# Performance work log

Measured on AMD Instinct MI355X. Metric: run time of the kernel, lower is better.

The kernel has to match this reference:

```python
import jax, jax.numpy as jnp
import numpy as np

NUM_OPS = 100_000
NUM_MACH = 512
H = 128
OPF = 6
MF = 2
L = 2
N_PREC = 800_000
N_CHALF = 800_000  # compat edges per direction
EPS = 1e-5


def setup_inputs() -> dict:
    key = jax.random.key(0)
    ks = jax.random.split(key, 20)
    op_features = jax.random.normal(ks[0], (NUM_OPS, OPF), dtype=jnp.float32)
    machine_features = jax.random.normal(ks[1], (NUM_MACH, MF), dtype=jnp.float32)
    prec_src = jax.random.randint(ks[2], (N_PREC,), 0, NUM_OPS, dtype=jnp.int32)
    prec_tgt = jax.random.randint(ks[3], (N_PREC,), 0, NUM_OPS, dtype=jnp.int32)
    precedence_edges = jnp.stack([prec_src, prec_tgt])  # [2, N_PREC]
    op_idx = jax.random.randint(ks[4], (N_CHALF,), 0, NUM_OPS, dtype=jnp.int32)
    m_idx = jax.random.randint(ks[5], (N_CHALF,), 0, NUM_MACH, dtype=jnp.int32)
    # bidirectional pairs in unified node space (machines offset by NUM_OPS)
    src = jnp.concatenate([op_idx, m_idx + NUM_OPS])
    tgt = jnp.concatenate([m_idx + NUM_OPS, op_idx])
    compatibility_edges = jnp.stack([src, tgt])  # [2, 2*N_CHALF]
    s = 0.05
    op_emb_W = jax.random.normal(ks[6], (H, OPF), dtype=jnp.float32) * s
    op_emb_b = jnp.zeros((H,), jnp.float32)
    mach_emb_W = jax.random.normal(ks[7], (H, MF), dtype=jnp.float32) * s
    mach_emb_b = jnp.zeros((H,), jnp.float32)
    prec_W = jax.random.normal(ks[8], (L, H, H), dtype=jnp.float32) * s
    prec_b = jax.random.normal(ks[9], (L, H), dtype=jnp.float32) * s
    compat_W = jax.random.normal(ks[10], (L, H, H), dtype=jnp.float32) * s
    compat_b = jax.random.normal(ks[11], (L, H), dtype=jnp.float32) * s
    op_ln_g = jnp.ones((L, H), jnp.float32)
    op_ln_b = jnp.zeros((L, H), jnp.float32)
    mach_ln_g = jnp.ones((L, H), jnp.float32)
    mach_ln_b = jnp.zeros((L, H), jnp.float32)
    return dict(op_features=op_features, machine_features=machine_features,
                precedence_edges=precedence_edges, compatibility_edges=compatibility_edges,
                op_emb_W=op_emb_W, op_emb_b=op_emb_b, mach_emb_W=mach_emb_W, mach_emb_b=mach_emb_b,
                prec_W=prec_W, prec_b=prec_b, compat_W=compat_W, compat_b=compat_b,
                op_ln_g=op_ln_g, op_ln_b=op_ln_b, mach_ln_g=mach_ln_g, mach_ln_b=mach_ln_b)


def _layer_norm(x, g, b):
    mu = jnp.mean(x, axis=-1, keepdims=True)
    var = jnp.mean(jnp.square(x - mu), axis=-1, keepdims=True)
    return (x - mu) * jax.lax.rsqrt(var + EPS) * g + b


def _scatter_mean(vals, idx, mask, n):
    # vals [E,H], idx [E], mask [E] bool (or None); mean over incoming edges, count clamped >= 1
    if mask is not None:
        vals = jnp.where(mask[:, None], vals, 0.0)
        idx = jnp.where(mask, idx, 0)
        ones = mask.astype(vals.dtype)
    else:
        ones = jnp.ones(idx.shape, vals.dtype)
    sums = jax.ops.segment_sum(vals, idx, num_segments=n)
    cnts = jax.ops.segment_sum(ones, idx, num_segments=n)
    return sums / jnp.maximum(cnts, 1.0)[:, None]


def _forward(op_features, machine_features, precedence_edges, compatibility_edges,
             op_emb_W, op_emb_b, mach_emb_W, mach_emb_b,
             prec_W, prec_b, compat_W, compat_b,
             op_ln_g, op_ln_b, mach_ln_g, mach_ln_b):
    num_ops = op_features.shape[0]
    num_mach = machine_features.shape[0]
    op_emb = op_features @ op_emb_W.T + op_emb_b
    mach_emb = machine_features @ mach_emb_W.T + mach_emb_b

    p_src, p_tgt = precedence_edges[0], precedence_edges[1]
    c_src, c_tgt = compatibility_edges[0], compatibility_edges[1]
    op2m = (c_src < num_ops) & (c_tgt >= num_ops)
    m2o = (c_src >= num_ops) & (c_tgt < num_ops)
    o2m_src = jnp.where(op2m, c_src, 0)
    o2m_tgt = jnp.where(op2m, c_tgt - num_ops, 0)
    m2o_src = jnp.where(m2o, c_src - num_ops, 0)
    m2o_tgt = jnp.where(m2o, c_tgt, 0)

    for l in range(L):
        # precedence (op -> op): linear-then-gather == gather-then-linear
        op_t = op_emb @ prec_W[l].T + prec_b[l]            # [num_ops, H]
        op_emb_prec = _scatter_mean(op_t[p_src], p_tgt, None, num_ops)
        # compatibility, shared linear for both directions
        op_c = op_emb @ compat_W[l].T + compat_b[l]        # [num_ops, H]
        mach_c = mach_emb @ compat_W[l].T + compat_b[l]    # [num_mach, H]
        mach_emb_compat = _scatter_mean(op_c[o2m_src], o2m_tgt, op2m, num_mach)
        op_emb_compat = _scatter_mean(mach_c[m2o_src], m2o_tgt, m2o, num_ops)
        op_emb = _layer_norm(op_emb + op_emb_prec + op_emb_compat, op_ln_g[l], op_ln_b[l])
        mach_emb = _layer_norm(mach_emb + mach_emb_compat, mach_ln_g[l], mach_ln_b[l])
    return op_emb, mach_emb


def reference(op_features, machine_features, precedence_edges, compatibility_edges,
              op_emb_W, op_emb_b, mach_emb_W, mach_emb_b,
              prec_W, prec_b, compat_W, compat_b,
              op_ln_g, op_ln_b, mach_ln_g, mach_ln_b):
    return _forward(op_features, machine_features, precedence_edges, compatibility_edges,
                    op_emb_W, op_emb_b, mach_emb_W, mach_emb_b,
                    prec_W, prec_b, compat_W, compat_b,
                    op_ln_g, op_ln_b, mach_ln_g, mach_ln_b)
```

## Files before the change

### kernel.cpp

```cpp
#include <hip/hip_runtime.h>
#include <hip/hip_bf16.h>

#define NUM_OPS   100000
#define NUM_MACH  512
#define HDIM      128
#define P1        100352
#define NHIST     200704
#define NBLK      196
#define NCOARSE   784
#define NBC       256
#define NBM       256
#define MHWORDS   (NUM_MACH * NBM)
#define NBLK_M    128
#define NBLK_T    (NBLK + NBLK_M)

typedef short short8 __attribute__((ext_vector_type(8)));
typedef unsigned short ushort8 __attribute__((ext_vector_type(8)));
typedef float floatx4 __attribute__((ext_vector_type(4)));

__device__ __forceinline__ unsigned short f2bf(float f) {
    unsigned u = __float_as_uint(f);
    unsigned r = (u + 0x7FFFu + ((u >> 16) & 1u)) >> 16;
    return (unsigned short)r;
}
__device__ __forceinline__ float bf2f(unsigned short u) {
    return __uint_as_float(((unsigned)u) << 16);
}

__global__ void k_prep(const float* __restrict__ Fo, const float* __restrict__ Fm,
                       const float* __restrict__ Wo, const float* __restrict__ bo,
                       const float* __restrict__ Wm, const float* __restrict__ bm,
                       const float* __restrict__ Wp, const float* __restrict__ Wc,
                       unsigned short* __restrict__ op_ebf,
                       float* __restrict__ mach_emb, unsigned short* __restrict__ mach_ebf,
                       unsigned short* __restrict__ Wb) {
    int idx = blockIdx.x * blockDim.x + threadIdx.x;
    if (idx < NUM_OPS * HDIM) {
        int r = idx >> 7, h = idx & 127;
        const float* f = Fo + (size_t)r * 6;
        const float* w = Wo + (size_t)h * 6;
        float s = bo[h];
#pragma unroll
        for (int i = 0; i < 6; ++i) s += f[i] * w[i];
        op_ebf[idx] = f2bf(s);
        return;
    }
    idx -= NUM_OPS * HDIM;
    if (idx < NUM_MACH * HDIM) {
        int r = idx >> 7, h = idx & 127;
        const float* f = Fm + (size_t)r * 2;
        const float* w = Wm + (size_t)h * 2;
        float s = bm[h] + f[0] * w[0] + f[1] * w[1];
        mach_emb[idx] = s;
        mach_ebf[idx] = f2bf(s);
        return;
    }
    idx -= NUM_MACH * HDIM;
    if (idx < 2 * 128 * 256) {
        int l = idx >> 15, h = (idx >> 8) & 127, k = idx & 255;
        float v = (k < 128) ? Wp[(size_t)l * 16384 + h * 128 + k]
                            : Wc[(size_t)l * 16384 + h * 128 + (k - 128)];
        Wb[idx] = f2bf(v);
    }
}

__global__ __launch_bounds__(256) void k_front(const int* __restrict__ prec_e, int nprec,
                                               const int* __restrict__ comp_e, int E, int M,
                                               int* __restrict__ chist_bh,
                                               int* __restrict__ mach_bh) {
    __shared__ int hc[NCOARSE];
    __shared__ int hm[NUM_MACH];
    for (int i = threadIdx.x; i < NCOARSE; i += 256) hc[i] = 0;
    for (int i = threadIdx.x; i < NUM_MACH; i += 256) hm[i] = 0;
    __syncthreads();
    int NT = nprec + E;
    int ch = (NT + NBC - 1) / NBC;
    int i0 = blockIdx.x * ch, i1 = min(NT, i0 + ch);
    for (int i = i0 + threadIdx.x; i < i1; i += 256) {
        int key;
        if (i < nprec) key = prec_e[nprec + i];
        else {
            int e = i - nprec;
            key = P1 + comp_e[e];
            atomicAdd(&hm[comp_e[E + e] - M], 1);
        }
        atomicAdd(&hc[key >> 8], 1);
    }
    __syncthreads();
    for (int i = threadIdx.x; i < NCOARSE; i += 256)
        chist_bh[i * NBC + blockIdx.x] = hc[i];
    for (int i = threadIdx.x; i < NUM_MACH; i += 256)
        mach_bh[i * NBC + blockIdx.x] = hm[i];
}

__global__ __launch_bounds__(256) void k_cfill(const int* __restrict__ prec_e, int nprec,
                                               const int* __restrict__ comp_e, int E, int M,
                                               const int* __restrict__ scan,
                                               int* __restrict__ pairs) {
    __shared__ int cur[NCOARSE];
    for (int i = threadIdx.x; i < NCOARSE; i += 256) cur[i] = scan[i * NBC + blockIdx.x];
    __syncthreads();
    int NT = nprec + E;
    int ch = (NT + NBC - 1) / NBC;
    int i0 = blockIdx.x * ch, i1 = min(NT, i0 + ch);
    for (int i = i0 + threadIdx.x; i < i1; i += 256) {
        int key, val;
        if (i < nprec) { key = prec_e[nprec + i]; val = prec_e[i]; }
        else { int e = i - nprec; key = P1 + comp_e[e]; val = comp_e[E + e] - M; }
        int pos = atomicAdd(&cur[key >> 8], 1);
        pairs[pos] = (val << 8) | (key & 255);
    }
}

__global__ __launch_bounds__(256) void k_blocksum(const int* __restrict__ arr, int* __restrict__ partial) {
    __shared__ int sh[256];
    int b = blockIdx.x, t = threadIdx.x;
    int4 v = *(const int4*)(arr + b * 1024 + t * 4);
    sh[t] = v.x + v.y + v.z + v.w;
    __syncthreads();
    for (int o = 128; o; o >>= 1) { if (t < o) sh[t] += sh[t + o]; __syncthreads(); }
    if (!t) partial[b] = sh[0];
}

__global__ __launch_bounds__(256) void k_scanpart(const int* __restrict__ partial,
                                                  int* __restrict__ block_off) {
    __shared__ int sh[256];
    int t = threadIdx.x;
    int seg0 = blockIdx.x ? NBLK : 0;
    int n    = blockIdx.x ? NBLK_M : NBLK;
    int v = (t < n) ? partial[seg0 + t] : 0;
    sh[t] = v; __syncthreads();
    for (int o = 1; o < 256; o <<= 1) {
        int x = (t >= o) ? sh[t - o] : 0; __syncthreads();
        sh[t] += x; __syncthreads();
    }
    if (t < n) block_off[seg0 + t] = sh[t] - v;
}

__global__ __launch_bounds__(256) void k_scanwrite(const int* __restrict__ arr,
                                                   const int* __restrict__ block_off,
                                                   int* __restrict__ rs) {
    __shared__ int sh[256];
    int b = blockIdx.x, t = threadIdx.x;
    int base_i = b * 1024 + t * 4;
    int4 v = *(const int4*)(arr + base_i);
    int tsum = v.x + v.y + v.z + v.w;
    sh[t] = tsum; __syncthreads();
    for (int o = 1; o < 256; o <<= 1) {
        int x = (t >= o) ? sh[t - o] : 0; __syncthreads();
        sh[t] += x; __syncthreads();
    }
    int off = block_off[b] + sh[t] - tsum;
    int4 r; r.x = off; r.y = off + v.x; r.z = off + v.x + v.y; r.w = off + v.x + v.y + v.z;
    *(int4*)(rs + base_i) = r;
}

__global__ __launch_bounds__(256) void k_finefill(const int* __restrict__ scans, int NT,
                                                  const int* __restrict__ pairs,
                                                  int* __restrict__ rs,
                                                  int* __restrict__ bucket_all,
                                                  const int* __restrict__ comp_e, int E, int M,
                                                  int* __restrict__ bucket_mach,
                                                  int* __restrict__ mach_rs) {
    int t = threadIdx.x;
    if (blockIdx.x < NCOARSE) {
        __shared__ int hh[256];
        __shared__ int ex[256];
        __shared__ int cu[256];
        int b = blockIdx.x;
        int s = scans[b * NBC];
        int e = (b == NCOARSE - 1) ? NT : scans[(b + 1) * NBC];
        hh[t] = 0;
        __syncthreads();
        for (int i = s + t; i < e; i += 256) atomicAdd(&hh[pairs[i] & 255], 1);
        __syncthreads();
        int v = hh[t];
        ex[t] = v; __syncthreads();
        for (int o = 1; o < 256; o <<= 1) {
            int x = (t >= o) ? ex[t - o] : 0; __syncthreads();
            ex[t] += x; __syncthreads();
        }
        int start = s + ex[t] - v;
        rs[b * 256 + t] = start;
        cu[t] = start;
        __syncthreads();
        for (int i = s + t; i < e; i += 256) {
            int p = pairs[i];
            int pos = atomicAdd(&cu[p & 255], 1);
            bucket_all[pos] = ((unsigned)p) >> 8;
        }
    } else {
        __shared__ int cur[NUM_MACH];
        int blk = blockIdx.x - NCOARSE;
        const int* moff = scans + NHIST;
        for (int i = t; i < NUM_MACH; i += 256) cur[i] = moff[i * NBM + blk];
        if (blk == 0) {
            for (int m = t; m < NUM_MACH; m += 256) mach_rs[m] = moff[m * NBM];
            if (t == 0) mach_rs[NUM_MACH] = E;
        }
        __syncthreads();
        int nprec = NT - E;
        int chNT = (NT + NBC - 1) / NBC;
        int e0 = blk * chNT - nprec;       if (e0 < 0) e0 = 0;
        int e1 = (blk + 1) * chNT - nprec; if (e1 > E) e1 = E;
        for (int e = e0 + t; e < e1; e += 256) {
            int m = comp_e[E + e] - M;
            int op = comp_e[e];
            int pos = atomicAdd(&cur[m], 1);
            bucket_mach[pos] = op;
        }
    }
}

#define ACC8(acc, v) { _Pragma("unroll") for (int k = 0; k < 8; ++k) acc[k] += bf2f((unsigned short)v[k]); }

__global__ __launch_bounds__(256) void k_aggmg(
    const unsigned short* __restrict__ op_ebf, const unsigned short* __restrict__ mach_ebf,
    const int* __restrict__ rs, const int* __restrict__ bucket_all,
    unsigned short* __restrict__ Ab, int* __restrict__ flags, int M,
    const int* __restrict__ mach_rs, const int* __restrict__ bucket_mach,
    float* __restrict__ mach_sum, int nb_agg) {
    int wave = threadIdx.x >> 6, lane = threadIdx.x & 63;
    int g = lane >> 4;
    int d = (lane & 15) * 8;

    if ((int)blockIdx.x < nb_agg) {
        int r = blockIdx.x * 4 + wave;
        if (r >= M) return;
        int sA = rs[r],      eA = rs[r + 1];
        int sB = rs[P1 + r], eB = rs[P1 + r + 1];

        float a[8], b[8];
#pragma unroll
        for (int k = 0; k < 8; ++k) { a[k] = 0.f; b[k] = 0.f; }

        int baseA = sA, baseB = sB;
        while (baseA < eA || baseB < eB) {
            int cA = (baseA < eA) ? min(64, eA - baseA) : 0;
            int cB = (baseB < eB) ? min(64, eB - baseB) : 0;
            int idxA = (lane < cA) ? bucket_all[baseA + lane] : 0;
            int idxB = (lane < cB) ? bucket_all[baseB + lane] : 0;
            int jm = max(cA, cB);
            for (int j = 0; j < jm; j += 8) {
                int j0 = j + g, j1 = j + 4 + g;
                int rA0 = __shfl(idxA, j0);
                int rA1 = __shfl(idxA, j1);
                int rB0 = __shfl(idxB, j0);
                int rB1 = __shfl(idxB, j1);
                short8 vA0 = *(const short8*)(op_ebf   + (size_t)rA0 * HDIM + d);
                short8 vA1 = *(const short8*)(op_ebf   + (size_t)rA1 * HDIM + d);
                short8 vB0 = *(const short8*)(mach_ebf + (size_t)rB0 * HDIM + d);
                short8 vB1 = *(const short8*)(mach_ebf + (size_t)rB1 * HDIM + d);
                if (j0 < cA) ACC8(a, vA0);
                if (j1 < cA) ACC8(a, vA1);
                if (j0 < cB) ACC8(b, vB0);
                if (j1 < cB) ACC8(b, vB1);
            }
            baseA += 64; baseB += 64;
        }
#pragma unroll
        for (int k = 0; k < 8; ++k) {
            a[k] += __shfl_xor(a[k], 16);
            a[k] += __shfl_xor(a[k], 32);
            b[k] += __shfl_xor(b[k], 16);
            b[k] += __shfl_xor(b[k], 32);
        }
        float pinv = 1.f / fmaxf((float)(eA - sA), 1.f);
        float cinv = 1.f / fmaxf((float)(eB - sB), 1.f);

        if (lane < 16) {
            ushort8 pa, pb;
#pragma unroll
            for (int k = 0; k < 8; ++k) { pa[k] = f2bf(a[k] * pinv); pb[k] = f2bf(b[k] * cinv); }
            *(ushort8*)(Ab + (size_t)r * 256 + d)       = pa;
            *(ushort8*)(Ab + (size_t)r * 256 + 128 + d) = pb;
        }
        if (lane == 0) flags[r] = (eA > sA ? 1 : 0) | (eB > sB ? 2 : 0);
        return;
    }

    int b2 = blockIdx.x - nb_agg;
    int m  = b2 & 511;
    int yq = b2 >> 9;
    int s0 = mach_rs[m], e0 = mach_rs[m + 1];
    float a[8];
#pragma unroll
    for (int k = 0; k < 8; ++k) a[k] = 0.f;

    for (int base = s0 + (yq * 4 + wave) * 64; base < e0; base += 1024) {
        int cnt = min(64, e0 - base);
        int idx = (lane < cnt) ? bucket_mach[base + lane] : 0;
        int j = 0;
        for (; j + 16 <= cnt; j += 16) {
            int r0 = __shfl(idx, j + g);
            int r1 = __shfl(idx, j + 4 + g);
            int r2 = __shfl(idx, j + 8 + g);
            int r3 = __shfl(idx, j + 12 + g);
            short8 v0 = *(const short8*)(op_ebf + (size_t)r0 * HDIM + d);
            short8 v1 = *(const short8*)(op_ebf + (size_t)r1 * HDIM + d);
            short8 v2 = *(const short8*)(op_ebf + (size_t)r2 * HDIM + d);
            short8 v3 = *(const short8*)(op_ebf + (size_t)r3 * HDIM + d);
            ACC8(a, v0); ACC8(a, v1); ACC8(a, v2); ACC8(a, v3);
        }
        for (; j < cnt; j += 4) {
            int jj = j + g;
            int rowi = __shfl(idx, jj);
            short8 v = *(const short8*)(op_ebf + (size_t)rowi * HDIM + d);
            if (jj < cnt) ACC8(a, v);
        }
    }
#pragma unroll
    for (int k = 0; k < 8; ++k) {
        a[k] += __shfl_xor(a[k], 16);
        a[k] += __shfl_xor(a[k], 32);
    }
    if (lane < 16) {
#pragma unroll
        for (int k = 0; k < 8; ++k)
            atomicAdd(&mach_sum[m * HDIM + d + k], a[k]);
    }
}

__global__ __launch_bounds__(256) void k_gemm_mupd(
    const unsigned short* __restrict__ Ab, const unsigned short* __restrict__ embb,
    const unsigned short* __restrict__ Wb,
    const float* __restrict__ bp, const float* __restrict__ bc,
    const int* __restrict__ flags,
    const float* __restrict__ g, const float* __restrict__ bt,
    float* __restrict__ dstf, unsigned short* __restrict__ dstb, int M, int nb_gemm,
    const float* __restrict__ mach_emb, float* __restrict__ mach_sum,
    const int* __restrict__ mach_rs,
    const float* __restrict__ Wc,
    const float* __restrict__ gm, const float* __restrict__ btm,
    float* __restrict__ mdst, unsigned short* __restrict__ mdstb) {
    if ((int)blockIdx.x >= nb_gemm) {
        __shared__ float row[HDIM];
        __shared__ float red[4];
        int m = blockIdx.x - nb_gemm, t = threadIdx.x;
        int cnt = mach_rs[m + 1] - mach_rs[m];
        float sc = (cnt > 0) ? 1.f / (float)cnt : 0.f;
        if (t < HDIM) {
            row[t] = mach_sum[m * HDIM + t] * sc;
            mach_sum[m * HDIM + t] = 0.f;
        }
        __syncthreads();
        float x = 0.f, s = 0.f, q = 0.f;
        if (t < HDIM) {
            float dot = bc[t];
            const float* w = Wc + (size_t)t * HDIM;
#pragma unroll 8
            for (int k = 0; k < HDIM; ++k) dot += row[k] * w[k];
            x = mach_emb[m * HDIM + t] + ((cnt > 0) ? dot : 0.f);
            s = x; q = x * x;
#pragma unroll
            for (int o = 32; o; o >>= 1) { s += __shfl_xor(s, o); q += __shfl_xor(q, o); }
            int wv = t >> 6;
            if ((t & 63) == 0) { red[wv * 2] = s; red[wv * 2 + 1] = q; }
        }
        __syncthreads();
        if (t < HDIM) {
            s = red[0] + red[2]; q = red[1] + red[3];
            float mu = s * (1.f / 128.f);
            float rstd = rsqrtf(fmaxf(q * (1.f / 128.f) - mu * mu, 0.f) + 1e-5f);
            float y = (x - mu) * rstd * gm[t] + btm[t];
            mdst[m * HDIM + t] = y;
            if (mdstb) mdstb[m * HDIM + t] = f2bf(y);
        }
        return;
    }

    int wave = threadIdx.x >> 6, lane = threadIdx.x & 63;
    int m0 = blockIdx.x * 64 + wave * 16;
    if (m0 >= M) return;
    int quad = lane >> 4, col = lane & 15;

    floatx4 acc[8];
#pragma unroll
    for (int t = 0; t < 8; ++t) acc[t] = (floatx4){0.f, 0.f, 0.f, 0.f};

    const short* Arow  = (const short*)(Ab + (size_t)(m0 + col) * 256);
    const short* Wbase = (const short*)Wb;

#pragma unroll
    for (int ks = 0; ks < 8; ++ks) {
        short8 a = *(const short8*)(Arow + ks * 32 + quad * 8);
#pragma unroll
        for (int t = 0; t < 8; ++t) {
            short8 b = *(const short8*)(Wbase + (size_t)(t * 16 + col) * 256 + ks * 32 + quad * 8);
            acc[t] = __builtin_amdgcn_mfma_f32_16x16x32_bf16(a, b, acc[t], 0, 0, 0);
        }
    }

    float bpv[8], bcv[8], gv[8], btv[8];
#pragma unroll
    for (int t = 0; t < 8; ++t) {
        int c = t * 16 + col;
        bpv[t] = bp[c]; bcv[t] = bc[c]; gv[t] = g[c]; btv[t] = bt[c];
    }
#pragma unroll
    for (int reg = 0; reg < 4; ++reg) {
        int r = m0 + quad * 4 + reg;
        int fl = flags[r];
        float fp = (fl & 1) ? 1.f : 0.f, fc = (fl & 2) ? 1.f : 0.f;
        float x[8]; float s = 0.f, q = 0.f;
#pragma unroll
        for (int t = 0; t < 8; ++t) {
            float v = acc[t][reg] + bf2f(embb[(size_t)r * HDIM + t * 16 + col]) + fp * bpv[t] + fc * bcv[t];
            x[t] = v; s += v; q += v * v;
        }
#pragma unroll
        for (int msk = 1; msk < 16; msk <<= 1) { s += __shfl_xor(s, msk); q += __shfl_xor(q, msk); }
        float mu = s * (1.f / 128.f);
        float rstd = rsqrtf(fmaxf(q * (1.f / 128.f) - mu * mu, 0.f) + 1e-5f);
#pragma unroll
        for (int t = 0; t < 8; ++t) {
            float y = (x[t] - mu) * rstd * gv[t] + btv[t];
            if (dstf) dstf[(size_t)r * HDIM + t * 16 + col] = y;
            if (dstb) dstb[(size_t)r * HDIM + t * 16 + col] = f2bf(y);
        }
    }
}

extern "C" void kernel_launch(void* const* d_in, const int* in_sizes, int n_in,
                              void* d_out, int out_size, void* d_ws, size_t ws_size,
                              hipStream_t stream) {
    const float* op_feat    = (const float*)d_in[0];
    const float* m_feat     = (const float*)d_in[1];
    const int*   prec_e     = (const int*)d_in[2];
    const int*   comp_e     = (const int*)d_in[3];
    const float* op_emb_W   = (const float*)d_in[4];
    const float* op_emb_b   = (const float*)d_in[5];
    const float* mach_emb_W = (const float*)d_in[6];
    const float* mach_emb_b = (const float*)d_in[7];
    const float* prec_W     = (const float*)d_in[8];
    const float* prec_b     = (const float*)d_in[9];
    const float* compat_W   = (const float*)d_in[10];
    const float* compat_b   = (const float*)d_in[11];
    const float* op_ln_g    = (const float*)d_in[12];
    const float* op_ln_b    = (const float*)d_in[13];
    const float* mach_ln_g  = (const float*)d_in[14];
    const float* mach_ln_b  = (const float*)d_in[15];
    float* out = (float*)d_out;

    const int M = NUM_OPS, NM = NUM_MACH;
    const int nprec = in_sizes[2] / 2;
    const int ncomp = in_sizes[3] / 2;
    const int E = ncomp / 2;
    const int NT = nprec + E;

    float* ws = (float*)d_ws;
    size_t o = 0;
    unsigned short* op_ebf = (unsigned short*)(ws + o); o += (size_t)M * 64;
    unsigned short* Ab = (unsigned short*)(ws + o); o += (size_t)M * 128;
    unsigned short* Wb = (unsigned short*)(ws + o); o += 32768;
    float* mach_emb = ws + o; o += (size_t)NM * HDIM;
    unsigned short* mach_ebf = (unsigned short*)(ws + o); o += (size_t)NM * 64;
    float* mach_sum = ws + o; o += (size_t)NM * HDIM;
    int* ip = (int*)(ws + o);
    size_t io = 0;
    int* hists     = ip + io; io += NHIST + MHWORDS;
    int* scans     = ip + io; io += NHIST + MHWORDS;
    int* rs        = ip + io; io += NHIST;
    int* mach_rs   = ip + io; io += NM + 8;
    int* partialT  = ip + io; io += 512;
    int* block_off = ip + io; io += 512;
    int* flags     = ip + io; io += M;
    int* pairs     = ip + io; io += (size_t)NT;
    int* bucket_all  = ip + io; io += (size_t)NT;
    int* bucket_mach = ip + io; io += (size_t)E;

    int* mach_bh = hists + NHIST;

    k_front<<<NBC, 256, 0, stream>>>(prec_e, nprec, comp_e, E, M, hists, mach_bh);
    k_blocksum<<<NBLK_T, 256, 0, stream>>>(hists, partialT);
    k_scanpart<<<2, 256, 0, stream>>>(partialT, block_off);
    k_scanwrite<<<NBLK_T, 256, 0, stream>>>(hists, block_off, scans);
    k_cfill<<<NBC, 256, 0, stream>>>(prec_e, nprec, comp_e, E, M, scans, pairs);
    k_finefill<<<NCOARSE + NBM, 256, 0, stream>>>(scans, NT, pairs, rs, bucket_all,
                                                  comp_e, E, M, bucket_mach, mach_rs);

    int prep_total = (M + NM) * HDIM + 2 * 128 * 256;
    k_prep<<<(prep_total + 255) / 256, 256, 0, stream>>>(
        op_feat, m_feat, op_emb_W, op_emb_b, mach_emb_W, mach_emb_b,
        prec_W, compat_W, op_ebf, mach_emb, mach_ebf, Wb);
    hipMemsetAsync(mach_sum, 0, (size_t)NM * HDIM * sizeof(float), stream);

    const int nb_agg = (M + 3) / 4;
    const int nb_gemm = (M + 63) / 64;
    for (int l = 0; l < 2; ++l) {
        int last = (l == 1);
        const float* bpl = prec_b   + (size_t)l * HDIM;
        const float* Wc  = compat_W + (size_t)l * HDIM * HDIM;
        const float* bcl = compat_b + (size_t)l * HDIM;

        k_aggmg<<<nb_agg + NM * 4, 256, 0, stream>>>(
            op_ebf, mach_ebf, rs, bucket_all, Ab, flags, M,
            mach_rs, bucket_mach, mach_sum, nb_agg);

        k_gemm_mupd<<<nb_gemm + NM, 256, 0, stream>>>(
            Ab, op_ebf, Wb + (size_t)l * 128 * 256, bpl, bcl, flags,
            op_ln_g + (size_t)l * HDIM, op_ln_b + (size_t)l * HDIM,
            last ? out : nullptr, last ? nullptr : op_ebf, M, nb_gemm,
            mach_emb, mach_sum, mach_rs, Wc,
            mach_ln_g + (size_t)l * HDIM, mach_ln_b + (size_t)l * HDIM,
            last ? (out + (size_t)M * HDIM) : mach_emb, last ? nullptr : mach_ebf);
    }
}
```

Baseline: 529.2 us.

## Fuse CSR build and prep kernels into one cooperative kernel with grid syncs

```diff
diff --git a/kernel.cpp b/kernel.cpp
--- a/kernel.cpp
+++ b/kernel.cpp
@@ -1,5 +1,8 @@
 #include <hip/hip_runtime.h>
 #include <hip/hip_bf16.h>
+#include <hip/hip_cooperative_groups.h>
+
+namespace cg = cooperative_groups;
 
 #define NUM_OPS   100000
 #define NUM_MACH  512
@@ -13,6 +16,7 @@
 #define MHWORDS   (NUM_MACH * NBM)
 #define NBLK_M    128
 #define NBLK_T    (NBLK + NBLK_M)
+#define NB_CSR    (NCOARSE + NBM)
 
 typedef short short8 __attribute__((ext_vector_type(8)));
 typedef unsigned short ushort8 __attribute__((ext_vector_type(8)));
@@ -27,147 +31,143 @@
     return __uint_as_float(((unsigned)u) << 16);
 }
 
-__global__ void k_prep(const float* __restrict__ Fo, const float* __restrict__ Fm,
-                       const float* __restrict__ Wo, const float* __restrict__ bo,
-                       const float* __restrict__ Wm, const float* __restrict__ bm,
-                       const float* __restrict__ Wp, const float* __restrict__ Wc,
-                       unsigned short* __restrict__ op_ebf,
-                       float* __restrict__ mach_emb, unsigned short* __restrict__ mach_ebf,
-                       unsigned short* __restrict__ Wb) {
-    int idx = blockIdx.x * blockDim.x + threadIdx.x;
-    if (idx < NUM_OPS * HDIM) {
-        int r = idx >> 7, h = idx & 127;
-        const float* f = Fo + (size_t)r * 6;
-        const float* w = Wo + (size_t)h * 6;
-        float s = bo[h];
-#pragma unroll
-        for (int i = 0; i < 6; ++i) s += f[i] * w[i];
-        op_ebf[idx] = f2bf(s);
-        return;
-    }
-    idx -= NUM_OPS * HDIM;
-    if (idx < NUM_MACH * HDIM) {
-        int r = idx >> 7, h = idx & 127;
-        const float* f = Fm + (size_t)r * 2;
-        const float* w = Wm + (size_t)h * 2;
-        float s = bm[h] + f[0] * w[0] + f[1] * w[1];
-        mach_emb[idx] = s;
-        mach_ebf[idx] = f2bf(s);
-        return;
-    }
-    idx -= NUM_MACH * HDIM;
-    if (idx < 2 * 128 * 256) {
-        int l = idx >> 15, h = (idx >> 8) & 127, k = idx & 255;
-        float v = (k < 128) ? Wp[(size_t)l * 16384 + h * 128 + k]
-                            : Wc[(size_t)l * 16384 + h * 128 + (k - 128)];
-        Wb[idx] = f2bf(v);
-    }
-}
-
-__global__ __launch_bounds__(256) void k_front(const int* __restrict__ prec_e, int nprec,
-                                               const int* __restrict__ comp_e, int E, int M,
-                                               int* __restrict__ chist_bh,
-                                               int* __restrict__ mach_bh) {
-    __shared__ int hc[NCOARSE];
-    __shared__ int hm[NUM_MACH];
-    for (int i = threadIdx.x; i < NCOARSE; i += 256) hc[i] = 0;
-    for (int i = threadIdx.x; i < NUM_MACH; i += 256) hm[i] = 0;
-    __syncthreads();
-    int NT = nprec + E;
-    int ch = (NT + NBC - 1) / NBC;
-    int i0 = blockIdx.x * ch, i1 = min(NT, i0 + ch);
-    for (int i = i0 + threadIdx.x; i < i1; i += 256) {
-        int key;
-        if (i < nprec) key = prec_e[nprec + i];
-        else {
-            int e = i - nprec;
-            key = P1 + comp_e[e];
-            atomicAdd(&hm[comp_e[E + e] - M], 1);
-        }
-        atomicAdd(&hc[key >> 8], 1);
-    }
-    __syncthreads();
-    for (int i = threadIdx.x; i < NCOARSE; i += 256)
-        chist_bh[i * NBC + blockIdx.x] = hc[i];
-    for (int i = threadIdx.x; i < NUM_MACH; i += 256)
-        mach_bh[i * NBC + blockIdx.x] = hm[i];
-}
-
-__global__ __launch_bounds__(256) void k_cfill(const int* __restrict__ prec_e, int nprec,
-                                               const int* __restrict__ comp_e, int E, int M,
-                                               const int* __restrict__ scan,
-                                               int* __restrict__ pairs) {
-    __shared__ int cur[NCOARSE];
-    for (int i = threadIdx.x; i < NCOARSE; i += 256) cur[i] = scan[i * NBC + blockIdx.x];
-    __syncthreads();
-    int NT = nprec + E;
-    int ch = (NT + NBC - 1) / NBC;
-    int i0 = blockIdx.x * ch, i1 = min(NT, i0 + ch);
-    for (int i = i0 + threadIdx.x; i < i1; i += 256) {
-        int key, val;
-        if (i < nprec) { key = prec_e[nprec + i]; val = prec_e[i]; }
-        else { int e = i - nprec; key = P1 + comp_e[e]; val = comp_e[E + e] - M; }
-        int pos = atomicAdd(&cur[key >> 8], 1);
-        pairs[pos] = (val << 8) | (key & 255);
-    }
-}
-
-__global__ __launch_bounds__(256) void k_blocksum(const int* __restrict__ arr, int* __restrict__ partial) {
-    __shared__ int sh[256];
+__global__ __launch_bounds__(256) void k_csr(
+    const int* __restrict__ prec_e, int nprec,
+    const int* __restrict__ comp_e, int E, int M, int NT,
+    int* __restrict__ hists, int* __restrict__ scans,
+    int* __restrict__ partialT, int* __restrict__ block_off,
+    int* __restrict__ pairs, int* __restrict__ rs,
+    int* __restrict__ bucket_all, int* __restrict__ bucket_mach,
+    int* __restrict__ mach_rs,
+    const float* __restrict__ Fo, const float* __restrict__ Fm,
+    const float* __restrict__ Wo, const float* __restrict__ bo,
+    const float* __restrict__ Wm, const float* __restrict__ bm,
+    const float* __restrict__ Wp, const float* __restrict__ Wc,
+    unsigned short* __restrict__ op_ebf, float* __restrict__ mach_emb,
+    unsigned short* __restrict__ mach_ebf, unsigned short* __restrict__ Wb,
+    float* __restrict__ mach_sum) {
+    cg::grid_group grid = cg::this_grid();
+    __shared__ int shm[NCOARSE + NUM_MACH];
     int b = blockIdx.x, t = threadIdx.x;
-    int4 v = *(const int4*)(arr + b * 1024 + t * 4);
-    sh[t] = v.x + v.y + v.z + v.w;
-    __syncthreads();
-    for (int o = 128; o; o >>= 1) { if (t < o) sh[t] += sh[t + o]; __syncthreads(); }
-    if (!t) partial[b] = sh[0];
-}
-
-__global__ __launch_bounds__(256) void k_scanpart(const int* __restrict__ partial,
-                                                  int* __restrict__ block_off) {
-    __shared__ int sh[256];
-    int t = threadIdx.x;
-    int seg0 = blockIdx.x ? NBLK : 0;
-    int n    = blockIdx.x ? NBLK_M : NBLK;
-    int v = (t < n) ? partial[seg0 + t] : 0;
-    sh[t] = v; __syncthreads();
-    for (int o = 1; o < 256; o <<= 1) {
-        int x = (t >= o) ? sh[t - o] : 0; __syncthreads();
-        sh[t] += x; __syncthreads();
-    }
-    if (t < n) block_off[seg0 + t] = sh[t] - v;
-}
-
-__global__ __launch_bounds__(256) void k_scanwrite(const int* __restrict__ arr,
-                                                   const int* __restrict__ block_off,
-                                                   int* __restrict__ rs) {
-    __shared__ int sh[256];
-    int b = blockIdx.x, t = threadIdx.x;
-    int base_i = b * 1024 + t * 4;
-    int4 v = *(const int4*)(arr + base_i);
-    int tsum = v.x + v.y + v.z + v.w;
-    sh[t] = tsum; __syncthreads();
-    for (int o = 1; o < 256; o <<= 1) {
-        int x = (t >= o) ? sh[t - o] : 0; __syncthreads();
-        sh[t] += x; __syncthreads();
-    }
-    int off = block_off[b] + sh[t] - tsum;
-    int4 r; r.x = off; r.y = off + v.x; r.z = off + v.x + v.y; r.w = off + v.x + v.y + v.z;
-    *(int4*)(rs + base_i) = r;
-}
-
-__global__ __launch_bounds__(256) void k_finefill(const int* __restrict__ scans, int NT,
-                                                  const int* __restrict__ pairs,
-                                                  int* __restrict__ rs,
-                                                  int* __restrict__ bucket_all,
-                                                  const int* __restrict__ comp_e, int E, int M,
-                                                  int* __restrict__ bucket_mach,
-                                                  int* __restrict__ mach_rs) {
-    int t = threadIdx.x;
-    if (blockIdx.x < NCOARSE) {
-        __shared__ int hh[256];
-        __shared__ int ex[256];
-        __shared__ int cu[256];
-        int b = blockIdx.x;
+    int* mach_bh = hists + NHIST;
+
+    if (b < NBC) {
+        int* hc = shm;
+        int* hm = shm + NCOARSE;
+        for (int i = t; i < NCOARSE; i += 256) hc[i] = 0;
+        for (int i = t; i < NUM_MACH; i += 256) hm[i] = 0;
+        __syncthreads();
+        int ch = (NT + NBC - 1) / NBC;
+        int i0 = b * ch, i1 = min(NT, i0 + ch);
+        for (int i = i0 + t; i < i1; i += 256) {
+            int key;
+            if (i < nprec) key = prec_e[nprec + i];
+            else {
+                int e = i - nprec;
+                key = P1 + comp_e[e];
+                atomicAdd(&hm[comp_e[E + e] - M], 1);
+            }
+            atomicAdd(&hc[key >> 8], 1);
+        }
+        __syncthreads();
+        for (int i = t; i < NCOARSE; i += 256) hists[i * NBC + b] = hc[i];
+        for (int i = t; i < NUM_MACH; i += 256) mach_bh[i * NBC + b] = hm[i];
+    } else {
+        const int T0 = NUM_OPS * HDIM;
+        const int T1 = T0 + NUM_MACH * HDIM;
+        const int T2 = T1 + 2 * 128 * 256;
+        const int T3 = T2 + NUM_MACH * HDIM;
+        int stride = (NB_CSR - NBC) * 256;
+        for (int idx = (b - NBC) * 256 + t; idx < T3; idx += stride) {
+            if (idx < T0) {
+                int r = idx >> 7, h = idx & 127;
+                const float* f = Fo + (size_t)r * 6;
+                const float* w = Wo + (size_t)h * 6;
+                float s = bo[h];
+#pragma unroll
+                for (int i = 0; i < 6; ++i) s += f[i] * w[i];
+                op_ebf[idx] = f2bf(s);
+            } else if (idx < T1) {
+                int j = idx - T0;
+                int r = j >> 7, h = j & 127;
+                const float* f = Fm + (size_t)r * 2;
+                const float* w = Wm + (size_t)h * 2;
+                float s = bm[h] + f[0] * w[0] + f[1] * w[1];
+                mach_emb[j] = s;
+                mach_ebf[j] = f2bf(s);
+            } else if (idx < T2) {
+                int j = idx - T1;
+                int l = j >> 15, h = (j >> 8) & 127, k = j & 255;
+                float v = (k < 128) ? Wp[(size_t)l * 16384 + h * 128 + k]
+                                    : Wc[(size_t)l * 16384 + h * 128 + (k - 128)];
+                Wb[j] = f2bf(v);
+            } else {
+                mach_sum[idx - T2] = 0.f;
+            }
+        }
+    }
+    grid.sync();
+
+    if (b < NBLK_T) {
+        int* sh = shm;
+        int4 v = *(const int4*)(hists + b * 1024 + t * 4);
+        sh[t] = v.x + v.y + v.z + v.w;
+        __syncthreads();
+        for (int o = 128; o; o >>= 1) { if (t < o) sh[t] += sh[t + o]; __syncthreads(); }
+        if (!t) partialT[b] = sh[0];
+    }
+    grid.sync();
+
+    if (b < 2) {
+        int* sh = shm;
+        int seg0 = b ? NBLK : 0;
+        int n    = b ? NBLK_M : NBLK;
+        int v = (t < n) ? partialT[seg0 + t] : 0;
+        sh[t] = v; __syncthreads();
+        for (int o = 1; o < 256; o <<= 1) {
+            int x = (t >= o) ? sh[t - o] : 0; __syncthreads();
+            sh[t] += x; __syncthreads();
+        }
+        if (t < n) block_off[seg0 + t] = sh[t] - v;
+    }
+    grid.sync();
+
+    if (b < NBLK_T) {
+        int* sh = shm;
+        int base_i = b * 1024 + t * 4;
+        int4 v = *(const int4*)(hists + base_i);
+        int tsum = v.x + v.y + v.z + v.w;
+        sh[t] = tsum; __syncthreads();
+        for (int o = 1; o < 256; o <<= 1) {
+            int x = (t >= o) ? sh[t - o] : 0; __syncthreads();
+            sh[t] += x; __syncthreads();
+        }
+        int off = block_off[b] + sh[t] - tsum;
+        int4 r; r.x = off; r.y = off + v.x; r.z = off + v.x + v.y; r.w = off + v.x + v.y + v.z;
+        *(int4*)(scans + base_i) = r;
+    }
+    grid.sync();
+
+    if (b < NBC) {
+        int* cur = shm;
+        for (int i = t; i < NCOARSE; i += 256) cur[i] = scans[i * NBC + b];
+        __syncthreads();
+        int ch = (NT + NBC - 1) / NBC;
+        int i0 = b * ch, i1 = min(NT, i0 + ch);
+        for (int i = i0 + t; i < i1; i += 256) {
+            int key, val;
+            if (i < nprec) { key = prec_e[nprec + i]; val = prec_e[i]; }
+            else { int e = i - nprec; key = P1 + comp_e[e]; val = comp_e[E + e] - M; }
+            int pos = atomicAdd(&cur[key >> 8], 1);
+            pairs[pos] = (val << 8) | (key & 255);
+        }
+    }
+    grid.sync();
+
+    if (b < NCOARSE) {
+        int* hh = shm;
+        int* ex = shm + 256;
+        int* cu = shm + 512;
         int s = scans[b * NBC];
         int e = (b == NCOARSE - 1) ? NT : scans[(b + 1) * NBC];
         hh[t] = 0;
@@ -190,8 +190,8 @@
             bucket_all[pos] = ((unsigned)p) >> 8;
         }
     } else {
-        __shared__ int cur[NUM_MACH];
-        int blk = blockIdx.x - NCOARSE;
+        int* cur = shm;
+        int blk = b - NCOARSE;
         const int* moff = scans + NHIST;
         for (int i = t; i < NUM_MACH; i += 256) cur[i] = moff[i * NBM + blk];
         if (blk == 0) {
@@ -199,7 +199,6 @@
             if (t == 0) mach_rs[NUM_MACH] = E;
         }
         __syncthreads();
-        int nprec = NT - E;
         int chNT = (NT + NBC - 1) / NBC;
         int e0 = blk * chNT - nprec;       if (e0 < 0) e0 = 0;
         int e1 = (blk + 1) * chNT - nprec; if (e1 > E) e1 = E;
@@ -424,10 +423,10 @@
 extern "C" void kernel_launch(void* const* d_in, const int* in_sizes, int n_in,
                               void* d_out, int out_size, void* d_ws, size_t ws_size,
                               hipStream_t stream) {
+    const int*   prec_e     = (const int*)d_in[2];
+    const int*   comp_e     = (const int*)d_in[3];
     const float* op_feat    = (const float*)d_in[0];
     const float* m_feat     = (const float*)d_in[1];
-    const int*   prec_e     = (const int*)d_in[2];
-    const int*   comp_e     = (const int*)d_in[3];
     const float* op_emb_W   = (const float*)d_in[4];
     const float* op_emb_b   = (const float*)d_in[5];
     const float* mach_emb_W = (const float*)d_in[6];
@@ -442,11 +441,12 @@
     const float* mach_ln_b  = (const float*)d_in[15];
     float* out = (float*)d_out;
 
-    const int M = NUM_OPS, NM = NUM_MACH;
-    const int nprec = in_sizes[2] / 2;
+    int M = NUM_OPS;
+    const int NM = NUM_MACH;
+    int nprec = in_sizes[2] / 2;
     const int ncomp = in_sizes[3] / 2;
-    const int E = ncomp / 2;
-    const int NT = nprec + E;
+    int E = ncomp / 2;
+    int NT = nprec + E;
 
     float* ws = (float*)d_ws;
     size_t o = 0;
@@ -469,21 +469,14 @@
     int* bucket_all  = ip + io; io += (size_t)NT;
     int* bucket_mach = ip + io; io += (size_t)E;
 
-    int* mach_bh = hists + NHIST;
-
-    k_front<<<NBC, 256, 0, stream>>>(prec_e, nprec, comp_e, E, M, hists, mach_bh);
-    k_blocksum<<<NBLK_T, 256, 0, stream>>>(hists, partialT);
-    k_scanpart<<<2, 256, 0, stream>>>(partialT, block_off);
-    k_scanwrite<<<NBLK_T, 256, 0, stream>>>(hists, block_off, scans);
-    k_cfill<<<NBC, 256, 0, stream>>>(prec_e, nprec, comp_e, E, M, scans, pairs);
-    k_finefill<<<NCOARSE + NBM, 256, 0, stream>>>(scans, NT, pairs, rs, bucket_all,
-                                                  comp_e, E, M, bucket_mach, mach_rs);
-
-    int prep_total = (M + NM) * HDIM + 2 * 128 * 256;
-    k_prep<<<(prep_total + 255) / 256, 256, 0, stream>>>(
-        op_feat, m_feat, op_emb_W, op_emb_b, mach_emb_W, mach_emb_b,
-        prec_W, compat_W, op_ebf, mach_emb, mach_ebf, Wb);
-    hipMemsetAsync(mach_sum, 0, (size_t)NM * HDIM * sizeof(float), stream);
+    void* csr_args[] = {
+        (void*)&prec_e, (void*)&nprec, (void*)&comp_e, (void*)&E, (void*)&M, (void*)&NT,
+        (void*)&hists, (void*)&scans, (void*)&partialT, (void*)&block_off,
+        (void*)&pairs, (void*)&rs, (void*)&bucket_all, (void*)&bucket_mach, (void*)&mach_rs,
+        (void*)&op_feat, (void*)&m_feat, (void*)&op_emb_W, (void*)&op_emb_b,
+        (void*)&mach_emb_W, (void*)&mach_emb_b, (void*)&prec_W, (void*)&compat_W,
+        (void*)&op_ebf, (void*)&mach_emb, (void*)&mach_ebf, (void*)&Wb, (void*)&mach_sum };
+    hipLaunchCooperativeKernel((void*)k_csr, dim3(NB_CSR), dim3(256), csr_args, 0, stream);
 
     const int nb_agg = (M + 3) / 4;
     const int nb_gemm = (M + 63) / 64;
```

Measured after the change: 1.128 ms. 2.13x slower.
